# Kernel optimization log

Hardware: AMD Instinct MI355X
Metric: run time of the kernel (lower is better)

The kernel has to match this reference:

```python
import jax, jax.numpy as jnp
import numpy as np

N = 4096; E = 65536; F_IN = 500; H = 64; RATIO = 0.8
K1 = int(np.ceil(RATIO * N))      # 3277
K2 = int(np.ceil(RATIO * K1))     # 2622
K3 = int(np.ceil(RATIO * K2))     # 2098


def _dense_adj(edge_index, n):
    # A[dst, src] = 1 for each edge (PyG source->target flow), then add_remaining_self_loops
    A = jnp.zeros((n, n), jnp.float32).at[edge_index[1], edge_index[0]].set(1.0)
    return A.at[jnp.diag_indices(n)].set(1.0)


def _gcn(A, x, W, b):
    # GCNConv: D^-1/2 (A + I) D^-1/2 @ (x @ W) + b  (edge weights are all 1 here)
    n = A.shape[0]
    A = A.at[jnp.diag_indices(n)].set(1.0)
    d = A.sum(axis=1)
    dis = jnp.where(d > 0, jax.lax.rsqrt(d), 0.0)
    An = dis[:, None] * A * dis[None, :]
    return An @ (x @ W) + b


def _score(A, x, w_rel, b_rel, w_root):
    # SAGPooling default GraphConv scorer: W_rel * sum_j x_j + b_rel + W_root * x_i
    return ((A @ x) @ w_rel + b_rel + x @ w_root)[:, 0]


def _pool(A, x, s, k):
    # topk by score, gate kept features with tanh(score), filter adjacency to kept nodes
    vals, idx = jax.lax.top_k(s, k)
    return x[idx] * jnp.tanh(vals)[:, None], A[idx][:, idx], idx


def _augment(A):
    # augment_adj: spspmm(A, A) = A^2; edge weights are discarded so result is binary
    return (A @ A > 0).astype(A.dtype)


def setup_inputs() -> dict:
    key = jax.random.key(0)
    ks = jax.random.split(key, 16)
    g = lambda k, shp: jax.random.normal(k, shp, jnp.float32) / np.sqrt(shp[0])
    z = lambda shp: jnp.zeros(shp, jnp.float32)
    return {
        "x": jax.random.normal(ks[0], (N, F_IN), jnp.float32),
        "w1": g(ks[1], (F_IN, H)), "b1": z((H,)),
        "w2": g(ks[2], (H, H)), "b2": z((H,)),
        "w3": g(ks[3], (H, H)), "b3": z((H,)),
        "p1_wrel": g(ks[4], (H, 1)), "p1_brel": z((1,)), "p1_wroot": g(ks[5], (H, 1)),
        "p2_wrel": g(ks[6], (H, 1)), "p2_brel": z((1,)), "p2_wroot": g(ks[7], (H, 1)),
        "p3_wrel": g(ks[8], (H, 1)), "p3_brel": z((1,)), "p3_wroot": g(ks[9], (H, 1)),
        "u0_w": g(ks[10], (H, H)), "u0_b": z((H,)),
        "u1_w": g(ks[11], (H, H)), "u1_b": z((H,)),
        "u2_w": g(ks[12], (H, F_IN)), "u2_b": z((F_IN,)),
        "edge_index": jax.random.randint(ks[13], (2, E), 0, N),
    }


def reference(x, w1, b1, w2, b2, w3, b3,
              p1_wrel, p1_brel, p1_wroot,
              p2_wrel, p2_brel, p2_wroot,
              p3_wrel, p3_brel, p3_wroot,
              u0_w, u0_b, u1_w, u1_b, u2_w, u2_b,
              edge_index):
    A0 = _dense_adj(edge_index, N)                 # edge_index + self loops
    # encoder: conv -> SAGPool -> augment (A^2), x3
    x1 = _gcn(A0, x, w1, b1)
    x1p, A1, perm1 = _pool(A0, x1, _score(A0, x1, p1_wrel, p1_brel, p1_wroot), K1)
    A1a = _augment(A1)
    x2 = _gcn(A1a, x1p, w2, b2)
    x2p, A2, perm2 = _pool(A1a, x2, _score(A1a, x2, p2_wrel, p2_brel, p2_wroot), K2)
    A2a = _augment(A2)
    x3 = _gcn(A2a, x2p, w3, b3)
    x3p, A3, perm3 = _pool(A2a, x3, _score(A2a, x3, p3_wrel, p3_brel, p3_wroot), K3)
    # decoder: scatter-unpool (up[perm] = z) then conv on the stored adjacency
    z = x3p
    up = jnp.zeros((K2, H), x.dtype).at[perm3].set(z)
    z = jax.nn.relu(_gcn(A2a, up, u0_w, u0_b))
    up = jnp.zeros((K1, H), x.dtype).at[perm2].set(z)
    z = jax.nn.relu(_gcn(A1a, up, u1_w, u1_b))
    up = jnp.zeros((N, H), x.dtype).at[perm1].set(z)
    z = _gcn(A0, up, u2_w, u2_b)
    return z
```

## Files before the change

### kernel.cpp

```cpp
#include <hip/hip_runtime.h>


constexpr int NN  = 4096;
constexpr int EE  = 65536;
constexpr int FIN = 500;
constexpr int KK1 = 3277, KK2 = 2622, KK3 = 2098;
constexpr int W0  = 128;
constexpr int W1  = (KK1 + 31) / 32;
constexpr int W2  = (KK2 + 31) / 32;
constexpr int CAP = 2048;


__global__ void fill4_kernel(float4* p, long n4) {
  long i = (long)blockIdx.x * blockDim.x + threadIdx.x;
  long stride = (long)gridDim.x * blockDim.x;
  float4 z = make_float4(0.f, 0.f, 0.f, 0.f);
  for (; i < n4; i += stride) p[i] = z;
}

__global__ void scatter_bits_kernel(unsigned* Ab, const int* __restrict__ ei) {
  int e = blockIdx.x * 256 + threadIdx.x;
  if (e < EE) {
    int src = ei[e], dst = ei[EE + e];
    atomicOr(&Ab[(size_t)dst * W0 + (src >> 5)], 1u << (src & 31));
  }
  if (e < NN) atomicOr(&Ab[(size_t)e * W0 + (e >> 5)], 1u << (e & 31));
}

__global__ void popcnt_dis_kernel(const unsigned* __restrict__ bits, int Wd,
                                  float* dis, int M) {
  int lane = threadIdx.x & 63;
  int row = blockIdx.x * 4 + (threadIdx.x >> 6);
  if (row >= M) return;
  const unsigned* rb = bits + (size_t)row * Wd;
  int c = 0;
  for (int w = lane; w < Wd; w += 64) c += __popc(rb[w]);
  for (int off = 32; off; off >>= 1) c += __shfl_down(c, off, 64);
  if (!lane) dis[row] = c > 0 ? rsqrtf((float)c) : 0.f;
}

__global__ void spmm_nbr_kernel(const unsigned* __restrict__ bits, int Wd,
                                const float* __restrict__ B,
                                const float* __restrict__ base,
                                const float* __restrict__ rowscale,
                                const float* __restrict__ bias,
                                const float* __restrict__ wrel,
                                const float* __restrict__ wroot,
                                float* __restrict__ tvec, float* __restrict__ rvec,
                                const int* __restrict__ sperm,
                                const float* __restrict__ sscale,
                                float* __restrict__ C, int M, int relu) {
  __shared__ int nbr[4][CAP];
  __shared__ int cnt[4];
  int lane = threadIdx.x & 63, wv = threadIdx.x >> 6;
  int row = blockIdx.x * 4 + wv;
  if (threadIdx.x < 4) cnt[threadIdx.x] = 0;
  __syncthreads();
  if (row < M) {
    const unsigned* rb = bits + (size_t)row * Wd;
    for (int w = lane; w < Wd; w += 64) {
      unsigned m = rb[w];
      while (m) {
        int b = __ffs(m) - 1;
        m &= m - 1;
        int idx = atomicAdd(&cnt[wv], 1);
        if (idx < CAP) nbr[wv][idx] = (w << 5) + b;
      }
    }
  }
  __syncthreads();
  if (row >= M) return;
  int nc = cnt[wv];
  float acc;
  if (nc <= CAP) {
    const int* lst = nbr[wv];
    float a0 = 0.f, a1 = 0.f, a2 = 0.f, a3 = 0.f;
    int q = 0;
    for (; q + 8 <= nc; q += 8) {
      int j0 = lst[q],     j1 = lst[q + 1], j2 = lst[q + 2], j3 = lst[q + 3];
      int j4 = lst[q + 4], j5 = lst[q + 5], j6 = lst[q + 6], j7 = lst[q + 7];
      float v0 = B[(size_t)j0 * 64 + lane], v1 = B[(size_t)j1 * 64 + lane];
      float v2 = B[(size_t)j2 * 64 + lane], v3 = B[(size_t)j3 * 64 + lane];
      float v4 = B[(size_t)j4 * 64 + lane], v5 = B[(size_t)j5 * 64 + lane];
      float v6 = B[(size_t)j6 * 64 + lane], v7 = B[(size_t)j7 * 64 + lane];
      a0 += v0 + v4; a1 += v1 + v5; a2 += v2 + v6; a3 += v3 + v7;
    }
    for (; q < nc; q++) a0 += B[(size_t)lst[q] * 64 + lane];
    acc = (a0 + a1) + (a2 + a3);
  } else {
    const unsigned* rb = bits + (size_t)row * Wd;
    float a = 0.f;
    for (int w = 0; w < Wd; w++) {
      unsigned m = rb[w];
      while (m) {
        int b = __ffs(m) - 1;
        m &= m - 1;
        a += B[(size_t)((w << 5) + b) * 64 + lane];
      }
    }
    acc = a;
  }
  if (base) acc = base[lane] - acc;
  float v = acc * rowscale[row];
  if (bias) v += bias[lane];
  if (relu) v = fmaxf(v, 0.f);
  if (sperm) {
    int p = sperm[row];
    C[(size_t)p * 64 + lane] = v * sscale[p];
  } else {
    C[(size_t)row * 64 + lane] = v;
  }
  if (wrel) {
    float t1 = v * wrel[lane], t2 = v * wroot[lane];
    for (int off = 32; off; off >>= 1) {
      t1 += __shfl_down(t1, off, 64);
      t2 += __shfl_down(t2, off, 64);
    }
    if (!lane) { tvec[row] = t1; rvec[row] = t2; }
  }
}

__global__ void matvec_bits_kernel(const unsigned* __restrict__ bits, int Wd,
                                   const float* __restrict__ t,
                                   const float* __restrict__ rv,
                                   const float* __restrict__ brel,
                                   const float* __restrict__ total,
                                   float* __restrict__ s, int M) {
  int lane = threadIdx.x & 63;
  int row = blockIdx.x * 4 + (threadIdx.x >> 6);
  if (row >= M) return;
  const unsigned* rb = bits + (size_t)row * Wd;
  float acc = 0.f;
  for (int w = lane; w < Wd; w += 64) {
    unsigned m = rb[w];
    while (m) {
      int b = __ffs(m) - 1;
      m &= m - 1;
      acc += t[(w << 5) + b];
    }
  }
  for (int off = 32; off; off >>= 1) acc += __shfl_down(acc, off, 64);
  if (!lane) {
    float r0 = total ? total[0] - acc : acc;
    s[row] = r0 + brel[0] + rv[row];
  }
}

__global__ void vec_total_kernel(const float* __restrict__ t, int n, float* tot) {
  __shared__ float red[256];
  float a = 0.f;
  for (int i = threadIdx.x; i < n; i += 256) a += t[i];
  red[threadIdx.x] = a;
  __syncthreads();
  for (int o = 128; o; o >>= 1) {
    if (threadIdx.x < o) red[threadIdx.x] += red[threadIdx.x + o];
    __syncthreads();
  }
  if (!threadIdx.x) tot[0] = red[0];
}

__global__ void topk_count_kernel(const float* __restrict__ s, int n, int* rank) {
  __shared__ float sh[512];
  int j0 = blockIdx.y * 512;
  for (int j = threadIdx.x; j < 512; j += 256) {
    int gj = j0 + j;
    sh[j] = gj < n ? s[gj] : 0.f;
  }
  __syncthreads();
  int i = blockIdx.x * 256 + threadIdx.x;
  if (i >= n) return;
  float si = s[i];
  int jmax = min(512, n - j0);
  int cnt = 0;
  for (int j = 0; j < jmax; j++) {
    float sj = sh[j];
    int gj = j0 + j;
    cnt += (sj > si || (sj == si && gj < i)) ? 1 : 0;
  }
  if (cnt) atomicAdd(&rank[i], cnt);
}

__global__ void topk_place_kernel(const float* __restrict__ s,
                                  const int* __restrict__ rank, int n, int k,
                                  int* perm, float* vals) {
  int i = blockIdx.x * 256 + threadIdx.x;
  if (i >= n) return;
  int rk = rank[i];
  if (rk < k) { perm[rk] = i; vals[rk] = s[i]; }
}

__global__ void scatter_gate_kernel(const float* __restrict__ X,
                                    const int* __restrict__ perm,
                                    const float* __restrict__ vals,
                                    const float* __restrict__ scale,
                                    float* up, int k) {
  int r = blockIdx.x * 4 + (threadIdx.x >> 6);
  int f = threadIdx.x & 63;
  if (r < k) {
    int p = perm[r];
    up[(size_t)p * 64 + f] = X[(size_t)p * 64 + f] * tanhf(vals[r]) * scale[p];
  }
}

__global__ void subgraph_bits_kernel(const unsigned* __restrict__ Ab, int WdIn,
                                     const int* __restrict__ perm, int K, int WdOut,
                                     unsigned* __restrict__ out) {
  __shared__ unsigned rowb[128];
  int r = blockIdx.x;
  const unsigned* src = Ab + (size_t)perm[r] * WdIn;
  for (int w = threadIdx.x; w < WdIn; w += 256) rowb[w] = src[w];
  __syncthreads();
  unsigned* ob = out + (size_t)r * WdOut;
  for (int c0 = 0; c0 < WdOut * 32; c0 += 256) {
    int c = c0 + threadIdx.x;
    bool pred = false;
    if (c < K) {
      int pc = perm[c];
      pred = (rowb[pc >> 5] >> (pc & 31)) & 1u;
    }
    unsigned long long m = __ballot(pred);
    if ((threadIdx.x & 63) == 0) {
      int wb = (c0 >> 5) + ((threadIdx.x >> 6) << 1);
      if (wb < WdOut)     ob[wb]     = (unsigned)m;
      if (wb + 1 < WdOut) ob[wb + 1] = (unsigned)(m >> 32);
    }
  }
}

__global__ void augment_or_kernel(const unsigned* __restrict__ in,
                                  unsigned* __restrict__ out,
                                  unsigned* __restrict__ holes,
                                  float* __restrict__ dis, int Wd, int K) {
  __shared__ unsigned roww[128];
  __shared__ int nbr[CAP];
  __shared__ int cnt;
  __shared__ int pcred[128];
  int i = blockIdx.x;
  if (threadIdx.x == 0) cnt = 0;
  const unsigned* rin = in + (size_t)i * Wd;
  for (int w = threadIdx.x; w < Wd; w += 128) roww[w] = rin[w];
  __syncthreads();
  for (int w = threadIdx.x; w < Wd; w += 128) {
    unsigned m = roww[w];
    while (m) {
      int b = __ffs(m) - 1;
      m &= m - 1;
      int idx = atomicAdd(&cnt, 1);
      if (idx < CAP) nbr[idx] = w * 32 + b;
    }
  }
  __syncthreads();
  int nc = min(cnt, CAP);
  int pc = 0;
  for (int w = threadIdx.x; w < Wd; w += 128) {
    unsigned a0 = 0, a1 = 0, a2 = 0, a3 = 0;
    int q = 0;
    for (; q + 4 <= nc; q += 4) {
      a0 |= in[(size_t)nbr[q] * Wd + w];
      a1 |= in[(size_t)nbr[q + 1] * Wd + w];
      a2 |= in[(size_t)nbr[q + 2] * Wd + w];
      a3 |= in[(size_t)nbr[q + 3] * Wd + w];
    }
    for (; q < nc; q++) a0 |= in[(size_t)nbr[q] * Wd + w];
    unsigned acc = (a0 | a1) | (a2 | a3);
    pc += __popc(acc);
    if (out) out[(size_t)i * Wd + w] = acc;
    if (holes) {
      int valid = K - w * 32;
      unsigned mask = valid >= 32 ? 0xffffffffu : ((1u << valid) - 1u);
      holes[(size_t)i * Wd + w] = ~acc & mask;
    }
  }
  pcred[threadIdx.x] = pc;
  __syncthreads();
  for (int o = 64; o; o >>= 1) {
    if (threadIdx.x < o) pcred[threadIdx.x] += pcred[threadIdx.x + o];
    __syncthreads();
  }
  if (!threadIdx.x) dis[i] = pcred[0] > 0 ? rsqrtf((float)pcred[0]) : 0.f;
}

__global__ void gemm_feat_kernel(const float* __restrict__ A, int lda,
                                 const float* __restrict__ B,
                                 const float* __restrict__ rowscale,
                                 float* __restrict__ C, int M, int K) {
  __shared__ float Bs[64][65];
  __shared__ float As[4][64];
  int lane = threadIdx.x & 63, wv = threadIdx.x >> 6;
  int row = blockIdx.x * 4 + wv;
  float acc = 0.f;
  for (int k0 = 0; k0 < K; k0 += 64) {
    for (int l = threadIdx.x; l < 64 * 64; l += 256) {
      int kk = l >> 6, ff = l & 63;
      int gk = k0 + kk;
      Bs[kk][ff] = gk < K ? B[(size_t)gk * 64 + ff] : 0.f;
    }
    int gk = k0 + lane;
    As[wv][lane] = (row < M && gk < K) ? A[(size_t)row * lda + gk] : 0.f;
    __syncthreads();
    if (row < M) {
#pragma unroll 16
      for (int kk = 0; kk < 64; kk++) acc += As[wv][kk] * Bs[kk][lane];
    }
    __syncthreads();
  }
  if (row < M) {
    float v = acc;
    if (rowscale) v *= rowscale[row];
    C[(size_t)row * 64 + lane] = v;
  }
}

__global__ void gemm_k64_kernel(const float* __restrict__ X,
                                const float* __restrict__ B,
                                const int* __restrict__ perm,
                                const float* __restrict__ vals,
                                const float* __restrict__ gscale,
                                float* __restrict__ C, int M) {
  __shared__ float Bs[64][65];
  __shared__ float As[4][64];
  int lane = threadIdx.x & 63, wv = threadIdx.x >> 6;
  int row = blockIdx.x * 4 + wv;
  for (int l = threadIdx.x; l < 64 * 64; l += 256) Bs[l >> 6][l & 63] = B[l];
  if (row < M) {
    int src = row;
    float g = 1.f;
    if (perm) {
      src = perm[row];
      g = tanhf(vals[row]) * gscale[row];
    }
    As[wv][lane] = X[(size_t)src * 64 + lane] * g;
  }
  __syncthreads();
  if (row < M) {
    float acc = 0.f;
#pragma unroll 16
    for (int k = 0; k < 64; k++) acc += As[wv][k] * Bs[k][lane];
    C[(size_t)row * 64 + lane] = acc;
  }
}

__global__ void colsum_part_kernel(const float* __restrict__ X, int K,
                                   float* part) {
  __shared__ float red[4][64];
  int lane = threadIdx.x & 63, wv = threadIdx.x >> 6;
  int r0 = blockIdx.x * 64;
  float a = 0.f;
  for (int i = wv; i < 64; i += 4) {
    int r = r0 + i;
    if (r < K) a += X[(size_t)r * 64 + lane];
  }
  red[wv][lane] = a;
  __syncthreads();
  if (!wv)
    part[(size_t)blockIdx.x * 64 + lane] =
        red[0][lane] + red[1][lane] + red[2][lane] + red[3][lane];
}

__global__ void colsum_final_kernel(const float* __restrict__ part, int G,
                                    float* csum) {
  __shared__ float red[4][64];
  int lane = threadIdx.x & 63, wv = threadIdx.x >> 6;
  float a = 0.f;
  for (int g = wv; g < G; g += 4) a += part[(size_t)g * 64 + lane];
  red[wv][lane] = a;
  __syncthreads();
  if (!wv)
    csum[lane] = red[0][lane] + red[1][lane] + red[2][lane] + red[3][lane];
}

__global__ void gemm_wide4_kernel(const float* __restrict__ Y,
                                  const float* __restrict__ B,
                                  const float* __restrict__ bias,
                                  float* __restrict__ C, int M) {
  __shared__ float Ys[4][64];
  int r0 = blockIdx.x * 4;
  {
    int l = threadIdx.x;
    int r = l >> 6, k = l & 63;
    Ys[r][k] = (r0 + r < M) ? Y[(size_t)(r0 + r) * 64 + k] : 0.f;
  }
  __syncthreads();
  for (int c = threadIdx.x; c < FIN; c += 256) {
    float bv0 = bias[c];
    float a0 = bv0, a1 = bv0, a2 = bv0, a3 = bv0;
#pragma unroll 16
    for (int k = 0; k < 64; k++) {
      float bv = B[k * FIN + c];
      a0 += Ys[0][k] * bv;
      a1 += Ys[1][k] * bv;
      a2 += Ys[2][k] * bv;
      a3 += Ys[3][k] * bv;
    }
    if (r0 + 0 < M) C[(size_t)(r0 + 0) * FIN + c] = a0;
    if (r0 + 1 < M) C[(size_t)(r0 + 1) * FIN + c] = a1;
    if (r0 + 2 < M) C[(size_t)(r0 + 2) * FIN + c] = a2;
    if (r0 + 3 < M) C[(size_t)(r0 + 3) * FIN + c] = a3;
  }
}


extern "C" void kernel_launch(void* const* d_in, const int* in_sizes, int n_in,
                              void* d_out, int out_size, void* d_ws, size_t ws_size,
                              hipStream_t stream) {
  const float* x      = (const float*)d_in[0];
  const float* w1     = (const float*)d_in[1];
  const float* b1     = (const float*)d_in[2];
  const float* w2     = (const float*)d_in[3];
  const float* b2     = (const float*)d_in[4];
  const float* w3     = (const float*)d_in[5];
  const float* b3     = (const float*)d_in[6];
  const float* p1wrel = (const float*)d_in[7];
  const float* p1brel = (const float*)d_in[8];
  const float* p1wroot= (const float*)d_in[9];
  const float* p2wrel = (const float*)d_in[10];
  const float* p2brel = (const float*)d_in[11];
  const float* p2wroot= (const float*)d_in[12];
  const float* p3wrel = (const float*)d_in[13];
  const float* p3brel = (const float*)d_in[14];
  const float* p3wroot= (const float*)d_in[15];
  const float* u0w    = (const float*)d_in[16];
  const float* u0b    = (const float*)d_in[17];
  const float* u1w    = (const float*)d_in[18];
  const float* u1b    = (const float*)d_in[19];
  const float* u2w    = (const float*)d_in[20];
  const float* u2b    = (const float*)d_in[21];
  const int*   ei     = (const int*)d_in[22];
  float* out = (float*)d_out;

  char* wp = (char*)d_ws;
  auto alloc = [&](size_t bytes) -> void* {
    void* p = (void*)wp;
    wp += (bytes + 255) & ~(size_t)255;
    return p;
  };
  unsigned* A0b  = (unsigned*)alloc((size_t)NN  * W0 * 4);
  unsigned* A1b  = (unsigned*)alloc((size_t)KK1 * W1 * 4);
  unsigned* A1ab = (unsigned*)alloc((size_t)KK1 * W1 * 4);
  unsigned* A2b  = (unsigned*)alloc((size_t)KK2 * W2 * 4);
  unsigned* H2b  = (unsigned*)alloc((size_t)KK2 * W2 * 4);
  float* dis0 = (float*)alloc((size_t)NN * 4);
  float* dis1 = (float*)alloc((size_t)KK1 * 4);
  float* dis2 = (float*)alloc((size_t)KK2 * 4);
  float* xw   = (float*)alloc((size_t)NN * 64 * 4);
  float* x1   = (float*)alloc((size_t)NN * 64 * 4);
  float* x2   = (float*)alloc((size_t)KK1 * 64 * 4);
  float* x3   = (float*)alloc((size_t)KK2 * 64 * 4);
  float* up0  = (float*)alloc((size_t)KK2 * 64 * 4);
  float* up1  = (float*)alloc((size_t)KK1 * 64 * 4);
  float* up2  = (float*)alloc((size_t)NN * 64 * 4);
  float* y0   = (float*)alloc((size_t)NN * 64 * 4);
  float* tvec = (float*)alloc((size_t)NN * 4);
  float* rvec = (float*)alloc((size_t)NN * 4);
  float* svec = (float*)alloc((size_t)NN * 4);
  float* vals = (float*)alloc((size_t)NN * 4);
  float* part = (float*)alloc((size_t)64 * 64 * 4);
  float* csum = (float*)alloc((size_t)64 * 4);
  float* tot  = (float*)alloc((size_t)4);
  int* rank  = (int*)alloc((size_t)NN * 4);
  int* perm1 = (int*)alloc((size_t)KK1 * 4);
  int* perm2 = (int*)alloc((size_t)KK2 * 4);
  int* perm3 = (int*)alloc((size_t)KK3 * 4);

  auto fill = [&](void* p, long n_floats) {
    long n4 = (n_floats + 3) / 4;
    int grid = (int)min((long)2048, (n4 + 255) / 256);
    fill4_kernel<<<grid, 256, 0, stream>>>((float4*)p, n4);
  };

  fill(A0b, (long)NN * W0);
  fill(up0, (long)KK2 * 64);
  fill(up1, (long)KK1 * 64);
  fill(up2, (long)NN * 64);

  scatter_bits_kernel<<<(EE + 255) / 256, 256, 0, stream>>>(A0b, ei);
  popcnt_dis_kernel<<<NN / 4, 256, 0, stream>>>(A0b, W0, dis0, NN);

  gemm_feat_kernel<<<NN / 4, 256, 0, stream>>>(x, FIN, w1, dis0, xw, NN, FIN);
  spmm_nbr_kernel<<<NN / 4, 256, 0, stream>>>(A0b, W0, xw, nullptr, dis0, b1,
      p1wrel, p1wroot, tvec, rvec, nullptr, nullptr, x1, NN, 0);
  matvec_bits_kernel<<<NN / 4, 256, 0, stream>>>(A0b, W0, tvec, rvec, p1brel, nullptr, svec, NN);
  fill(rank, NN);
  topk_count_kernel<<<dim3((NN + 255) / 256, (NN + 511) / 512), 256, 0, stream>>>(svec, NN, rank);
  topk_place_kernel<<<(NN + 255) / 256, 256, 0, stream>>>(svec, rank, NN, KK1, perm1, vals);
  subgraph_bits_kernel<<<KK1, 256, 0, stream>>>(A0b, W0, perm1, KK1, W1, A1b);
  augment_or_kernel<<<KK1, 128, 0, stream>>>(A1b, A1ab, nullptr, dis1, W1, KK1);

  gemm_k64_kernel<<<(KK1 + 3) / 4, 256, 0, stream>>>(x1, w2, perm1, vals, dis1, xw, KK1);
  spmm_nbr_kernel<<<(KK1 + 3) / 4, 256, 0, stream>>>(A1ab, W1, xw, nullptr, dis1, b2,
      p2wrel, p2wroot, tvec, rvec, nullptr, nullptr, x2, KK1, 0);
  matvec_bits_kernel<<<(KK1 + 3) / 4, 256, 0, stream>>>(A1ab, W1, tvec, rvec, p2brel, nullptr, svec, KK1);
  fill(rank, NN);
  topk_count_kernel<<<dim3((KK1 + 255) / 256, (KK1 + 511) / 512), 256, 0, stream>>>(svec, KK1, rank);
  topk_place_kernel<<<(KK1 + 255) / 256, 256, 0, stream>>>(svec, rank, KK1, KK2, perm2, vals);
  subgraph_bits_kernel<<<KK2, 256, 0, stream>>>(A1ab, W1, perm2, KK2, W2, A2b);
  augment_or_kernel<<<KK2, 128, 0, stream>>>(A2b, nullptr, H2b, dis2, W2, KK2);

  gemm_k64_kernel<<<(KK2 + 3) / 4, 256, 0, stream>>>(x2, w3, perm2, vals, dis2, xw, KK2);
  colsum_part_kernel<<<(KK2 + 63) / 64, 256, 0, stream>>>(xw, KK2, part);
  colsum_final_kernel<<<1, 256, 0, stream>>>(part, (KK2 + 63) / 64, csum);
  spmm_nbr_kernel<<<(KK2 + 3) / 4, 256, 0, stream>>>(H2b, W2, xw, csum, dis2, b3,
      p3wrel, p3wroot, tvec, rvec, nullptr, nullptr, x3, KK2, 0);
  vec_total_kernel<<<1, 256, 0, stream>>>(tvec, KK2, tot);
  matvec_bits_kernel<<<(KK2 + 3) / 4, 256, 0, stream>>>(H2b, W2, tvec, rvec, p3brel, tot, svec, KK2);
  fill(rank, NN);
  topk_count_kernel<<<dim3((KK2 + 255) / 256, (KK2 + 511) / 512), 256, 0, stream>>>(svec, KK2, rank);
  topk_place_kernel<<<(KK2 + 255) / 256, 256, 0, stream>>>(svec, rank, KK2, KK3, perm3, vals);
  scatter_gate_kernel<<<(KK3 + 3) / 4, 256, 0, stream>>>(x3, perm3, vals, dis2, up0, KK3);

  gemm_k64_kernel<<<(KK2 + 3) / 4, 256, 0, stream>>>(up0, u0w, nullptr, nullptr, nullptr, xw, KK2);
  colsum_part_kernel<<<(KK2 + 63) / 64, 256, 0, stream>>>(xw, KK2, part);
  colsum_final_kernel<<<1, 256, 0, stream>>>(part, (KK2 + 63) / 64, csum);
  spmm_nbr_kernel<<<(KK2 + 3) / 4, 256, 0, stream>>>(H2b, W2, xw, csum, dis2, u0b,
      nullptr, nullptr, nullptr, nullptr, perm2, dis1, up1, KK2, 1);

  gemm_k64_kernel<<<(KK1 + 3) / 4, 256, 0, stream>>>(up1, u1w, nullptr, nullptr, nullptr, xw, KK1);
  spmm_nbr_kernel<<<(KK1 + 3) / 4, 256, 0, stream>>>(A1ab, W1, xw, nullptr, dis1, u1b,
      nullptr, nullptr, nullptr, nullptr, perm1, dis0, up2, KK1, 1);

  spmm_nbr_kernel<<<NN / 4, 256, 0, stream>>>(A0b, W0, up2, nullptr, dis0, nullptr,
      nullptr, nullptr, nullptr, nullptr, nullptr, nullptr, y0, NN, 0);
  gemm_wide4_kernel<<<NN / 4, 256, 0, stream>>>(y0, u2w, u2b, out, NN);
}
```

Before: 402.9 us.

## Register-tile the dense GEMMs, split-K the input GEMM, and merge zero fills

Measured after the change: 1.071 ms. +165.8%, slower.

```diff
diff --git a/kernel.cpp b/kernel.cpp
--- a/kernel.cpp
+++ b/kernel.cpp
@@ -125,7 +125,8 @@
                                    const float* __restrict__ rv,
                                    const float* __restrict__ brel,
                                    const float* __restrict__ total,
-                                   float* __restrict__ s, int M) {
+                                   float* __restrict__ s,
+                                   int* __restrict__ rankz, int M) {
   int lane = threadIdx.x & 63;
   int row = blockIdx.x * 4 + (threadIdx.x >> 6);
   if (row >= M) return;
@@ -143,6 +144,7 @@
   if (!lane) {
     float r0 = total ? total[0] - acc : acc;
     s[row] = r0 + brel[0] + rv[row];
+    rankz[row] = 0;
   }
 }
 
@@ -280,64 +282,107 @@
   if (!threadIdx.x) dis[i] = pcred[0] > 0 ? rsqrtf((float)pcred[0]) : 0.f;
 }
 
-__global__ void gemm_feat_kernel(const float* __restrict__ A, int lda,
-                                 const float* __restrict__ B,
-                                 const float* __restrict__ rowscale,
-                                 float* __restrict__ C, int M, int K) {
+__global__ void gemm500_kernel(const float* __restrict__ A,
+                               const float* __restrict__ B,
+                               float* __restrict__ part) {
+  __shared__ float As[32][68];
+  __shared__ float Bs[32][68];
+  int tr = threadIdx.x >> 4, tc = threadIdx.x & 15;
+  int row0 = blockIdx.x * 64;
+  int k0 = blockIdx.y * 125;
+  float acc[4][4] = {};
+  for (int c0 = 0; c0 < 125; c0 += 32) {
+    for (int l = threadIdx.x; l < 64 * 32; l += 256) {
+      int r = l >> 5, kk = l & 31;
+      int gk = c0 + kk;
+      As[kk][r] = (gk < 125) ? A[(size_t)(row0 + r) * FIN + k0 + gk] : 0.f;
+    }
+    for (int l = threadIdx.x; l < 32 * 64; l += 256) {
+      int kk = l >> 6, c = l & 63;
+      int gk = c0 + kk;
+      Bs[kk][c] = (gk < 125) ? B[(size_t)(k0 + gk) * 64 + c] : 0.f;
+    }
+    __syncthreads();
+#pragma unroll
+    for (int kk = 0; kk < 32; kk++) {
+      float4 av = *(const float4*)&As[kk][tr * 4];
+      float4 bv = *(const float4*)&Bs[kk][tc * 4];
+      float a[4] = {av.x, av.y, av.z, av.w};
+      float b[4] = {bv.x, bv.y, bv.z, bv.w};
+#pragma unroll
+      for (int i = 0; i < 4; i++)
+#pragma unroll
+        for (int j = 0; j < 4; j++) acc[i][j] += a[i] * b[j];
+    }
+    __syncthreads();
+  }
+  float* P = part + (size_t)blockIdx.y * NN * 64;
+#pragma unroll
+  for (int i = 0; i < 4; i++) {
+    float4 st = make_float4(acc[i][0], acc[i][1], acc[i][2], acc[i][3]);
+    *(float4*)&P[(size_t)(row0 + tr * 4 + i) * 64 + tc * 4] = st;
+  }
+}
+
+__global__ void reduce4_scale_kernel(const float4* __restrict__ part,
+                                     const float* __restrict__ rowscale,
+                                     float4* __restrict__ outp) {
+  int e = blockIdx.x * 256 + threadIdx.x;
+  if (e >= NN * 16) return;
+  float4 v0 = part[e];
+  float4 v1 = part[e + NN * 16];
+  float4 v2 = part[e + 2 * NN * 16];
+  float4 v3 = part[e + 3 * NN * 16];
+  float s = rowscale[e >> 4];
+  float4 r;
+  r.x = (v0.x + v1.x + v2.x + v3.x) * s;
+  r.y = (v0.y + v1.y + v2.y + v3.y) * s;
+  r.z = (v0.z + v1.z + v2.z + v3.z) * s;
+  r.w = (v0.w + v1.w + v2.w + v3.w) * s;
+  outp[e] = r;
+}
+
+__global__ void gemm_k64x4_kernel(const float* __restrict__ X,
+                                  const float* __restrict__ B,
+                                  const int* __restrict__ perm,
+                                  const float* __restrict__ vals,
+                                  const float* __restrict__ gscale,
+                                  float* __restrict__ C, int M) {
   __shared__ float Bs[64][65];
-  __shared__ float As[4][64];
-  int lane = threadIdx.x & 63, wv = threadIdx.x >> 6;
-  int row = blockIdx.x * 4 + wv;
-  float acc = 0.f;
-  for (int k0 = 0; k0 < K; k0 += 64) {
-    for (int l = threadIdx.x; l < 64 * 64; l += 256) {
-      int kk = l >> 6, ff = l & 63;
-      int gk = k0 + kk;
-      Bs[kk][ff] = gk < K ? B[(size_t)gk * 64 + ff] : 0.f;
-    }
-    int gk = k0 + lane;
-    As[wv][lane] = (row < M && gk < K) ? A[(size_t)row * lda + gk] : 0.f;
-    __syncthreads();
+  __shared__ float As2[64][20];
+  __shared__ int   srcs[16];
+  __shared__ float gates[16];
+  int t = threadIdx.x;
+  int c = t & 63, g = t >> 6;
+  int r0 = blockIdx.x * 16;
+  if (t < 16) {
+    int row = r0 + t;
+    int src = 0; float gt = 1.f;
     if (row < M) {
-#pragma unroll 16
-      for (int kk = 0; kk < 64; kk++) acc += As[wv][kk] * Bs[kk][lane];
-    }
-    __syncthreads();
-  }
-  if (row < M) {
-    float v = acc;
-    if (rowscale) v *= rowscale[row];
-    C[(size_t)row * 64 + lane] = v;
-  }
-}
-
-__global__ void gemm_k64_kernel(const float* __restrict__ X,
-                                const float* __restrict__ B,
-                                const int* __restrict__ perm,
-                                const float* __restrict__ vals,
-                                const float* __restrict__ gscale,
-                                float* __restrict__ C, int M) {
-  __shared__ float Bs[64][65];
-  __shared__ float As[4][64];
-  int lane = threadIdx.x & 63, wv = threadIdx.x >> 6;
-  int row = blockIdx.x * 4 + wv;
-  for (int l = threadIdx.x; l < 64 * 64; l += 256) Bs[l >> 6][l & 63] = B[l];
-  if (row < M) {
-    int src = row;
-    float g = 1.f;
-    if (perm) {
-      src = perm[row];
-      g = tanhf(vals[row]) * gscale[row];
-    }
-    As[wv][lane] = X[(size_t)src * 64 + lane] * g;
-  }
-  __syncthreads();
-  if (row < M) {
-    float acc = 0.f;
-#pragma unroll 16
-    for (int k = 0; k < 64; k++) acc += As[wv][k] * Bs[k][lane];
-    C[(size_t)row * 64 + lane] = acc;
-  }
+      src = row;
+      if (perm) { src = perm[row]; gt = tanhf(vals[row]) * gscale[row]; }
+    }
+    srcs[t] = src; gates[t] = gt;
+  }
+  for (int l = t; l < 64 * 64; l += 256) Bs[l >> 6][l & 63] = B[l];
+  __syncthreads();
+  for (int l = t; l < 16 * 64; l += 256) {
+    int rr = l >> 6, k = l & 63;
+    int p = (rr & 3) * 4 + (rr >> 2);
+    As2[k][p] = (r0 + rr < M) ? X[(size_t)srcs[rr] * 64 + k] * gates[rr] : 0.f;
+  }
+  __syncthreads();
+  float a0 = 0.f, a1 = 0.f, a2 = 0.f, a3 = 0.f;
+#pragma unroll
+  for (int k = 0; k < 64; k++) {
+    float4 av = *(const float4*)&As2[k][g * 4];
+    float bv = Bs[k][c];
+    a0 += av.x * bv; a1 += av.y * bv; a2 += av.z * bv; a3 += av.w * bv;
+  }
+  if (r0 + g      < M) C[(size_t)(r0 + g)      * 64 + c] = a0;
+  if (r0 + g + 4  < M) C[(size_t)(r0 + g + 4)  * 64 + c] = a1;
+  if (r0 + g + 8  < M) C[(size_t)(r0 + g + 8)  * 64 + c] = a2;
+  if (r0 + g + 12 < M) C[(size_t)(r0 + g + 12) * 64 + c] = a3;
 }
 
 __global__ void colsum_part_kernel(const float* __restrict__ X, int K,
@@ -369,33 +414,44 @@
     csum[lane] = red[0][lane] + red[1][lane] + red[2][lane] + red[3][lane];
 }
 
-__global__ void gemm_wide4_kernel(const float* __restrict__ Y,
-                                  const float* __restrict__ B,
-                                  const float* __restrict__ bias,
-                                  float* __restrict__ C, int M) {
-  __shared__ float Ys[4][64];
-  int r0 = blockIdx.x * 4;
-  {
-    int l = threadIdx.x;
+__global__ void gemm_wide_tile_kernel(const float* __restrict__ Y,
+                                      const float* __restrict__ W,
+                                      const float* __restrict__ bias,
+                                      float* __restrict__ C) {
+  __shared__ float Ys[64][68];
+  __shared__ float Ws[64][68];
+  int tr = threadIdx.x >> 4, tc = threadIdx.x & 15;
+  int row0 = blockIdx.x * 64, c0 = blockIdx.y * 64;
+  for (int l = threadIdx.x; l < 64 * 64; l += 256) {
     int r = l >> 6, k = l & 63;
-    Ys[r][k] = (r0 + r < M) ? Y[(size_t)(r0 + r) * 64 + k] : 0.f;
-  }
-  __syncthreads();
-  for (int c = threadIdx.x; c < FIN; c += 256) {
-    float bv0 = bias[c];
-    float a0 = bv0, a1 = bv0, a2 = bv0, a3 = bv0;
-#pragma unroll 16
-    for (int k = 0; k < 64; k++) {
-      float bv = B[k * FIN + c];
-      a0 += Ys[0][k] * bv;
-      a1 += Ys[1][k] * bv;
-      a2 += Ys[2][k] * bv;
-      a3 += Ys[3][k] * bv;
-    }
-    if (r0 + 0 < M) C[(size_t)(r0 + 0) * FIN + c] = a0;
-    if (r0 + 1 < M) C[(size_t)(r0 + 1) * FIN + c] = a1;
-    if (r0 + 2 < M) C[(size_t)(r0 + 2) * FIN + c] = a2;
-    if (r0 + 3 < M) C[(size_t)(r0 + 3) * FIN + c] = a3;
+    Ys[k][r] = Y[(size_t)(row0 + r) * 64 + k];
+  }
+  for (int l = threadIdx.x; l < 64 * 64; l += 256) {
+    int k = l >> 6, cc = l & 63;
+    int gc = c0 + cc;
+    Ws[k][cc] = gc < FIN ? W[(size_t)k * FIN + gc] : 0.f;
+  }
+  __syncthreads();
+  float acc[4][4] = {};
+#pragma unroll
+  for (int kk = 0; kk < 64; kk++) {
+    float4 av = *(const float4*)&Ys[kk][tr * 4];
+    float4 bv = *(const float4*)&Ws[kk][tc * 4];
+    float a[4] = {av.x, av.y, av.z, av.w};
+    float b[4] = {bv.x, bv.y, bv.z, bv.w};
+#pragma unroll
+    for (int i = 0; i < 4; i++)
+#pragma unroll
+      for (int j = 0; j < 4; j++) acc[i][j] += a[i] * b[j];
+  }
+#pragma unroll
+  for (int i = 0; i < 4; i++) {
+    int row = row0 + tr * 4 + i;
+#pragma unroll
+    for (int j = 0; j < 4; j++) {
+      int gc = c0 + tc * 4 + j;
+      if (gc < FIN) C[(size_t)row * FIN + gc] = acc[i][j] + bias[gc];
+    }
   }
 }
 
@@ -435,6 +491,10 @@
     return p;
   };
   unsigned* A0b  = (unsigned*)alloc((size_t)NN  * W0 * 4);
+  float* up0  = (float*)alloc((size_t)KK2 * 64 * 4);
+  float* up1  = (float*)alloc((size_t)KK1 * 64 * 4);
+  float* up2  = (float*)alloc((size_t)NN * 64 * 4);
+  char* zero_end = wp;
   unsigned* A1b  = (unsigned*)alloc((size_t)KK1 * W1 * 4);
   unsigned* A1ab = (unsigned*)alloc((size_t)KK1 * W1 * 4);
   unsigned* A2b  = (unsigned*)alloc((size_t)KK2 * W2 * 4);
@@ -446,10 +506,8 @@
   float* x1   = (float*)alloc((size_t)NN * 64 * 4);
   float* x2   = (float*)alloc((size_t)KK1 * 64 * 4);
   float* x3   = (float*)alloc((size_t)KK2 * 64 * 4);
-  float* up0  = (float*)alloc((size_t)KK2 * 64 * 4);
-  float* up1  = (float*)alloc((size_t)KK1 * 64 * 4);
-  float* up2  = (float*)alloc((size_t)NN * 64 * 4);
   float* y0   = (float*)alloc((size_t)NN * 64 * 4);
+  float* part500 = (float*)alloc((size_t)4 * NN * 64 * 4);
   float* tvec = (float*)alloc((size_t)NN * 4);
   float* rvec = (float*)alloc((size_t)NN * 4);
   float* svec = (float*)alloc((size_t)NN * 4);
@@ -462,63 +520,56 @@
   int* perm2 = (int*)alloc((size_t)KK2 * 4);
   int* perm3 = (int*)alloc((size_t)KK3 * 4);
 
-  auto fill = [&](void* p, long n_floats) {
-    long n4 = (n_floats + 3) / 4;
-    int grid = (int)min((long)2048, (n4 + 255) / 256);
-    fill4_kernel<<<grid, 256, 0, stream>>>((float4*)p, n4);
-  };
-
-  fill(A0b, (long)NN * W0);
-  fill(up0, (long)KK2 * 64);
-  fill(up1, (long)KK1 * 64);
-  fill(up2, (long)NN * 64);
+  {
+    long n4 = (long)(zero_end - (char*)A0b) / 16;
+    fill4_kernel<<<2048, 256, 0, stream>>>((float4*)A0b, n4);
+  }
 
   scatter_bits_kernel<<<(EE + 255) / 256, 256, 0, stream>>>(A0b, ei);
   popcnt_dis_kernel<<<NN / 4, 256, 0, stream>>>(A0b, W0, dis0, NN);
 
-  gemm_feat_kernel<<<NN / 4, 256, 0, stream>>>(x, FIN, w1, dis0, xw, NN, FIN);
+  gemm500_kernel<<<dim3(64, 4), 256, 0, stream>>>(x, w1, part500);
+  reduce4_scale_kernel<<<NN * 16 / 256, 256, 0, stream>>>(
+      (const float4*)part500, dis0, (float4*)xw);
   spmm_nbr_kernel<<<NN / 4, 256, 0, stream>>>(A0b, W0, xw, nullptr, dis0, b1,
       p1wrel, p1wroot, tvec, rvec, nullptr, nullptr, x1, NN, 0);
-  matvec_bits_kernel<<<NN / 4, 256, 0, stream>>>(A0b, W0, tvec, rvec, p1brel, nullptr, svec, NN);
-  fill(rank, NN);
+  matvec_bits_kernel<<<NN / 4, 256, 0, stream>>>(A0b, W0, tvec, rvec, p1brel, nullptr, svec, rank, NN);
   topk_count_kernel<<<dim3((NN + 255) / 256, (NN + 511) / 512), 256, 0, stream>>>(svec, NN, rank);
   topk_place_kernel<<<(NN + 255) / 256, 256, 0, stream>>>(svec, rank, NN, KK1, perm1, vals);
   subgraph_bits_kernel<<<KK1, 256, 0, stream>>>(A0b, W0, perm1, KK1, W1, A1b);
   augment_or_kernel<<<KK1, 128, 0, stream>>>(A1b, A1ab, nullptr, dis1, W1, KK1);
 
-  gemm_k64_kernel<<<(KK1 + 3) / 4, 256, 0, stream>>>(x1, w2, perm1, vals, dis1, xw, KK1);
+  gemm_k64x4_kernel<<<(KK1 + 15) / 16, 256, 0, stream>>>(x1, w2, perm1, vals, dis1, xw, KK1);
   spmm_nbr_kernel<<<(KK1 + 3) / 4, 256, 0, stream>>>(A1ab, W1, xw, nullptr, dis1, b2,
       p2wrel, p2wroot, tvec, rvec, nullptr, nullptr, x2, KK1, 0);
-  matvec_bits_kernel<<<(KK1 + 3) / 4, 256, 0, stream>>>(A1ab, W1, tvec, rvec, p2brel, nullptr, svec, KK1);
-  fill(rank, NN);
+  matvec_bits_kernel<<<(KK1 + 3) / 4, 256, 0, stream>>>(A1ab, W1, tvec, rvec, p2brel, nullptr, svec, rank, KK1);
   topk_count_kernel<<<dim3((KK1 + 255) / 256, (KK1 + 511) / 512), 256, 0, stream>>>(svec, KK1, rank);
   topk_place_kernel<<<(KK1 + 255) / 256, 256, 0, stream>>>(svec, rank, KK1, KK2, perm2, vals);
   subgraph_bits_kernel<<<KK2, 256, 0, stream>>>(A1ab, W1, perm2, KK2, W2, A2b);
   augment_or_kernel<<<KK2, 128, 0, stream>>>(A2b, nullptr, H2b, dis2, W2, KK2);
 
-  gemm_k64_kernel<<<(KK2 + 3) / 4, 256, 0, stream>>>(x2, w3, perm2, vals, dis2, xw, KK2);
+  gemm_k64x4_kernel<<<(KK2 + 15) / 16, 256, 0, stream>>>(x2, w3, perm2, vals, dis2, xw, KK2);
   colsum_part_kernel<<<(KK2 + 63) / 64, 256, 0, stream>>>(xw, KK2, part);
   colsum_final_kernel<<<1, 256, 0, stream>>>(part, (KK2 + 63) / 64, csum);
   spmm_nbr_kernel<<<(KK2 + 3) / 4, 256, 0, stream>>>(H2b, W2, xw, csum, dis2, b3,
       p3wrel, p3wroot, tvec, rvec, nullptr, nullptr, x3, KK2, 0);
   vec_total_kernel<<<1, 256, 0, stream>>>(tvec, KK2, tot);
-  matvec_bits_kernel<<<(KK2 + 3) / 4, 256, 0, stream>>>(H2b, W2, tvec, rvec, p3brel, tot, svec, KK2);
-  fill(rank, NN);
+  matvec_bits_kernel<<<(KK2 + 3) / 4, 256, 0, stream>>>(H2b, W2, tvec, rvec, p3brel, tot, svec, rank, KK2);
   topk_count_kernel<<<dim3((KK2 + 255) / 256, (KK2 + 511) / 512), 256, 0, stream>>>(svec, KK2, rank);
   topk_place_kernel<<<(KK2 + 255) / 256, 256, 0, stream>>>(svec, rank, KK2, KK3, perm3, vals);
   scatter_gate_kernel<<<(KK3 + 3) / 4, 256, 0, stream>>>(x3, perm3, vals, dis2, up0, KK3);
 
-  gemm_k64_kernel<<<(KK2 + 3) / 4, 256, 0, stream>>>(up0, u0w, nullptr, nullptr, nullptr, xw, KK2);
+  gemm_k64x4_kernel<<<(KK2 + 15) / 16, 256, 0, stream>>>(up0, u0w, nullptr, nullptr, nullptr, xw, KK2);
   colsum_part_kernel<<<(KK2 + 63) / 64, 256, 0, stream>>>(xw, KK2, part);
   colsum_final_kernel<<<1, 256, 0, stream>>>(part, (KK2 + 63) / 64, csum);
   spmm_nbr_kernel<<<(KK2 + 3) / 4, 256, 0, stream>>>(H2b, W2, xw, csum, dis2, u0b,
       nullptr, nullptr, nullptr, nullptr, perm2, dis1, up1, KK2, 1);
 
-  gemm_k64_kernel<<<(KK1 + 3) / 4, 256, 0, stream>>>(up1, u1w, nullptr, nullptr, nullptr, xw, KK1);
+  gemm_k64x4_kernel<<<(KK1 + 15) / 16, 256, 0, stream>>>(up1, u1w, nullptr, nullptr, nullptr, xw, KK1);
   spmm_nbr_kernel<<<(KK1 + 3) / 4, 256, 0, stream>>>(A1ab, W1, xw, nullptr, dis1, u1b,
       nullptr, nullptr, nullptr, nullptr, perm1, dis0, up2, KK1, 1);
 
   spmm_nbr_kernel<<<NN / 4, 256, 0, stream>>>(A0b, W0, up2, nullptr, dis0, nullptr,
       nullptr, nullptr, nullptr, nullptr, nullptr, nullptr, y0, NN, 0);
-  gemm_wide4_kernel<<<NN / 4, 256, 0, stream>>>(y0, u2w, u2b, out, NN);
-}
+  gemm_wide_tile_kernel<<<dim3(64, 8), 256, 0, stream>>>(y0, u2w, u2b, out);
+}
```
